# Performance work log

Measured on AMD Instinct MI355X. Metric: run time of the kernel, lower is better.

## Reference

```python
import jax, jax.numpy as jnp
import numpy as np

K = 4  # Chebyshev filter size (matches init_kwargs k)


def setup_inputs() -> dict:
    key = jax.random.key(0)
    ks = jax.random.split(key, 5)
    N, E, F_IN, F_OUT = 100000, 3200000, 128, 128
    signal = jax.random.normal(ks[0], (N, F_IN), dtype=jnp.float32)
    src = jax.random.randint(ks[1], (E,), 0, N, dtype=jnp.int32)
    dst = jax.random.randint(ks[2], (E,), 0, N, dtype=jnp.int32)
    W = jax.random.normal(ks[3], (F_OUT, F_IN * K), dtype=jnp.float32) * 0.02
    b = jax.random.normal(ks[4], (F_OUT,), dtype=jnp.float32) * 0.02
    lambda_max = jnp.ones((1,), dtype=jnp.float32) * 2.0
    return {"signal": signal, "src": src, "dst": dst, "W": W, "b": b,
            "lambda_max": lambda_max}


def reference(signal, src, dst, W, b, lambda_max):
    N = signal.shape[0]
    # in-degrees: number of edges landing on each node
    deg = jax.ops.segment_sum(jnp.ones_like(dst, dtype=signal.dtype), dst,
                              num_segments=N)
    d_sqrt = jnp.clip(deg, 1.0, None) ** -0.5  # [N]
    d_sqrt = d_sqrt[:, None]                   # [N, 1]

    def unn_laplacian(x):
        # D^{-1/2} A D^{-1/2} x via gather-scatter over edges
        msg = (x * d_sqrt)[src]                               # [E, F]
        agg = jax.ops.segment_sum(msg, dst, num_segments=N)   # [N, F]
        return agg * d_sqrt

    re_norm = 2.0 / lambda_max  # [1], broadcasts over [N, F]

    X0 = signal
    Xt = [X0]
    if K > 1:
        h = unn_laplacian(X0)
        X1 = -re_norm * h + X0 * (re_norm - 1.0)
        Xt.append(X1)
        for _ in range(2, K):
            h = unn_laplacian(X1)
            Xi = -2.0 * re_norm * h + X1 * 2.0 * (re_norm - 1.0) - X0
            Xt.append(Xi)
            X1, X0 = Xi, X1
    feats = jnp.concatenate(Xt, axis=-1)  # [N, K*F_in]
    return feats @ W.T + b
```

## Files before the change

### kernel.cpp

```cpp
#include <hip/hip_runtime.h>

#define FEAT 128
#define YS 8.0f
#define YIS 0.125f
#define BSHIFT 7
#define MAXB 1024
#define BIN_CH 8192
#define CAP 8192

typedef __attribute__((ext_vector_type(8))) short bf16x8;
typedef __attribute__((ext_vector_type(4))) float f32x4;

__device__ __forceinline__ float2 upk_bf2(unsigned int p) {
    union { unsigned int u; float f; } a, b;
    a.u = p << 16;
    b.u = p & 0xffff0000u;
    return make_float2(a.f, b.f);
}
__device__ __forceinline__ unsigned short f2bf(float f) {
    union { float f; unsigned int u; } v;
    v.f = f;
    unsigned int b = v.u + 0x7fffu + ((v.u >> 16) & 1u);
    return (unsigned short)(b >> 16);
}
__device__ __forceinline__ unsigned int pk_bf2(float x, float y) {
    return (unsigned int)f2bf(x) | ((unsigned int)f2bf(y) << 16);
}

__global__ __launch_bounds__(1024) void bin_kernel(const int* __restrict__ src,
                                                   const int* __restrict__ dst,
                                                   int* __restrict__ bcnt,
                                                   unsigned int* __restrict__ tmp,
                                                   int E, int NB) {
    __shared__ int cnt[MAXB];
    __shared__ int base[MAXB];
    int t = threadIdx.x;
    for (int i = t; i < NB; i += 1024) cnt[i] = 0;
    __syncthreads();
    int start = blockIdx.x * BIN_CH;
    int n = E - start;
    if (n > BIN_CH) n = BIN_CH;
    for (int k = t; k < n; k += 1024) atomicAdd(&cnt[dst[start + k] >> BSHIFT], 1);
    __syncthreads();
    for (int i = t; i < NB; i += 1024) {
        int c = cnt[i];
        base[i] = c ? atomicAdd(&bcnt[i], c) : 0;
        cnt[i] = 0;
    }
    __syncthreads();
    for (int k = t; k < n; k += 1024) {
        int s = src[start + k], d = dst[start + k];
        int b = d >> BSHIFT;
        int off = atomicAdd(&cnt[b], 1);
        tmp[(size_t)b * CAP + base[b] + off] =
            ((unsigned int)(d & 127) << 24) | (unsigned int)s;
    }
}

__global__ __launch_bounds__(256) void bucket_kernel(
    const unsigned int* __restrict__ tmp, const int* __restrict__ bcnt,
    float* __restrict__ dsq, int* __restrict__ rstart, int* __restrict__ rend,
    int* __restrict__ ssrc, int N) {
    __shared__ int ldeg[128];
    __shared__ int lofs[128];
    int b = blockIdx.x;
    int t = threadIdx.x;
    int cnt = bcnt[b];
    if (t < 128) ldeg[t] = 0;
    __syncthreads();
    const unsigned int* tp = tmp + (size_t)b * CAP;
    for (int e = t; e < cnt; e += 256) atomicAdd(&ldeg[tp[e] >> 24], 1);
    __syncthreads();
    int node = (b << BSHIFT) + t;
    int v = 0, pv = 0;
    if (t < 128 && node < N) {
        v = ldeg[t];
        pv = (v + 7) & ~7;
    }
    if (t < 128) lofs[t] = pv;
    __syncthreads();
    for (int off = 1; off < 128; off <<= 1) {
        int add = (t < 128 && t >= off) ? lofs[t - off] : 0;
        __syncthreads();
        if (t < 128) lofs[t] += add;
        __syncthreads();
    }
    int myStart = 0;
    if (t < 128) {
        myStart = lofs[t] - pv;
        if (node < N) {
            dsq[node] = rsqrtf((float)(v < 1 ? 1 : v));
            rstart[node] = b * CAP + myStart;
            rend[node] = b * CAP + lofs[t];
        }
        ldeg[t] = myStart;
    }
    __syncthreads();
    int* sp = ssrc + (size_t)b * CAP;
    for (int e = t; e < cnt; e += 256) {
        unsigned int p = tp[e];
        int dl = p >> 24;
        int pos = atomicAdd(&ldeg[dl], 1);
        sp[pos] = (int)(p & 0xFFFFFFu);
    }
    __syncthreads();
    if (t < 128 && node < N) {
        for (int p = myStart + v; p < myStart + pv; p++) sp[p] = N;
    }
}

__global__ void prep_kernel(const float* __restrict__ signal, const float* __restrict__ dsq,
                            unsigned int* __restrict__ X0b, unsigned short* __restrict__ y0,
                            unsigned short* __restrict__ y1, int total ) {
    int t = blockIdx.x * blockDim.x + threadIdx.x;
    if (t < 64) {
        y0[total + t] = 0;
        y1[total + t] = 0;
    }
    if (t >= total) return;
    int node = t >> 6;
    float2 v = ((const float2*)signal)[t];
    float ds = dsq[node];
    X0b[t] = pk_bf2(v.x, v.y);
    int p = __builtin_amdgcn_cvt_pk_fp8_f32(v.x * ds * YS, v.y * ds * YS, 0, false);
    y0[t] = (unsigned short)p;
}

__global__ void wconv_kernel(const float* __restrict__ W, unsigned int* __restrict__ Wb2,
                             int total ) {
    int u = blockIdx.x * blockDim.x + threadIdx.x;
    if (u >= total) return;
    int e2 = u & 3;
    int l15 = (u >> 2) & 15;
    int kg = (u >> 6) & 3;
    int kq = (u >> 8) & 3;
    int chunk = (u >> 10) & 3;
    int nt = (u >> 12) & 7;
    int col = nt * 16 + l15;
    int k = chunk * 128 + kq * 32 + kg * 8 + e2 * 2;
    float2 v = ((const float2*)W)[col * 256 + (k >> 1)];
    Wb2[u] = pk_bf2(v.x, v.y);
}

__global__ __launch_bounds__(256) void pull_combine_kernel(
    const unsigned short* __restrict__ y8, const int* __restrict__ rstart,
    const int* __restrict__ rend, const int* __restrict__ ssrc,
    const float* __restrict__ dsq, const unsigned int* __restrict__ xprev,
    const unsigned int* __restrict__ xpp, const float* __restrict__ lam,
    unsigned int* __restrict__ Xout, unsigned short* __restrict__ yout,
    int N, int mode) {
    int node = (blockIdx.x << 2) + (threadIdx.x >> 6);
    if (node >= N) return;
    int lane = threadIdx.x & 63;
    int i = __builtin_amdgcn_readfirstlane(rstart[node]);
    int end = __builtin_amdgcn_readfirstlane(rend[node]);
    float ax = 0.f, ay = 0.f;
    for (; i < end; i += 8) {
        int s[8];
#pragma unroll
        for (int j = 0; j < 8; j++) s[j] = __builtin_amdgcn_readfirstlane(ssrc[i + j]);
        unsigned int u[8];
#pragma unroll
        for (int j = 0; j < 8; j++) u[j] = y8[(size_t)s[j] * 64 + lane];
#pragma unroll
        for (int j = 0; j < 8; j++) {
            auto f = __builtin_amdgcn_cvt_pk_f32_fp8((int)u[j], false);
            ax += f[0];
            ay += f[1];
        }
    }
    float r = 2.0f / lam[0];
    float ds = dsq[node];
    size_t idx = (size_t)node * 64 + lane;
    float2 xp = upk_bf2(xprev[idx]);
    float rx, ry;
    if (mode == 1) {
        float alpha = -r * ds * YIS, beta = r - 1.0f;
        rx = alpha * ax + beta * xp.x;
        ry = alpha * ay + beta * xp.y;
    } else {
        float alpha = -2.0f * r * ds * YIS, beta = 2.0f * (r - 1.0f);
        float2 xq = upk_bf2(xpp[idx]);
        rx = alpha * ax + beta * xp.x - xq.x;
        ry = alpha * ay + beta * xp.y - xq.y;
    }
    Xout[idx] = pk_bf2(rx, ry);
    if (yout) {
        int p = __builtin_amdgcn_cvt_pk_fp8_f32(rx * ds * YS, ry * ds * YS, 0, false);
        yout[idx] = (unsigned short)p;
    }
}

__global__ __launch_bounds__(256, 4) void mfma_gemm_kernel(
    const unsigned short* __restrict__ X0, const unsigned short* __restrict__ X1,
    const unsigned short* __restrict__ X2, const unsigned short* __restrict__ X3,
    const unsigned short* __restrict__ Wb2, const float* __restrict__ bias,
    float* __restrict__ out, int M) {
    int tid = threadIdx.x;
    int lane = tid & 63;
    int w = tid >> 6;
    int m0 = blockIdx.x * 128 + w * 32;
    int l15 = lane & 15;
    int kg = lane >> 4;

    f32x4 acc[2][8];
#pragma unroll
    for (int rg = 0; rg < 2; rg++)
#pragma unroll
        for (int nt = 0; nt < 8; nt++) acc[rg][nt] = (f32x4)(0.f);

    const unsigned short* Xs[4] = {X0, X1, X2, X3};
    int arow[2];
#pragma unroll
    for (int rg = 0; rg < 2; rg++) {
        int r = m0 + rg * 16 + l15;
        arow[rg] = r < M ? r : M - 1;
    }
    const unsigned short* wlane = Wb2 + (kg * 16 + l15) * 8;

#pragma unroll
    for (int chunk = 0; chunk < 4; ++chunk) {
        const unsigned short* A = Xs[chunk];
#pragma unroll
        for (int kq = 0; kq < 4; kq++) {
            bf16x8 af[2];
#pragma unroll
            for (int rg = 0; rg < 2; rg++)
                af[rg] = *(const bf16x8*)(A + (size_t)arow[rg] * 128 + kq * 32 + kg * 8);
#pragma unroll
            for (int nt = 0; nt < 8; nt++) {
                bf16x8 bf = *(const bf16x8*)(wlane + nt * 8192 + chunk * 2048 + kq * 512);
#pragma unroll
                for (int rg = 0; rg < 2; rg++)
                    acc[rg][nt] = __builtin_amdgcn_mfma_f32_16x16x32_bf16(af[rg], bf,
                                                                          acc[rg][nt], 0, 0, 0);
            }
        }
    }
#pragma unroll
    for (int nt = 0; nt < 8; nt++) {
        int col = nt * 16 + l15;
        float bb = bias[col];
#pragma unroll
        for (int rg = 0; rg < 2; rg++) {
#pragma unroll
            for (int r = 0; r < 4; r++) {
                int row = m0 + rg * 16 + kg * 4 + r;
                if (row < M) out[(size_t)row * 128 + col] = acc[rg][nt][r] + bb;
            }
        }
    }
}

extern "C" void kernel_launch(void* const* d_in, const int* in_sizes, int n_in,
                              void* d_out, int out_size, void* d_ws, size_t ws_size,
                              hipStream_t stream) {
    const float* signal = (const float*)d_in[0];
    const int* src = (const int*)d_in[1];
    const int* dst = (const int*)d_in[2];
    const float* W = (const float*)d_in[3];
    const float* bias = (const float*)d_in[4];
    const float* lam = (const float*)d_in[5];
    int N = in_sizes[0] / FEAT;
    int E = in_sizes[1];
    float* out = (float*)d_out;
    int NB = (N + (1 << BSHIFT) - 1) >> BSHIFT;

    char* ws = (char*)d_ws;
    size_t off = 0;
    auto alloc = [&](size_t bytes) {
        char* p = ws + off;
        off += (bytes + 511) & ~(size_t)511;
        return p;
    };
    size_t nodeBf = (size_t)N * FEAT * 2;
    size_t nodeF8 = (size_t)(N + 1) * FEAT;
    size_t bucketBytes = (size_t)NB * CAP * 4;

    float* dsq = (float*)alloc((size_t)N * 4);
    int* bcnt = (int*)alloc((size_t)NB * 4);
    int* rstart = (int*)alloc((size_t)N * 4);
    int* rend = (int*)alloc((size_t)N * 4);
    int* ssrc = (int*)alloc(bucketBytes);
    unsigned int* tmp = (unsigned int*)alloc(bucketBytes);
    unsigned int* Wb = (unsigned int*)alloc((size_t)128 * 512 * 2);
    unsigned int* X0b = (unsigned int*)alloc(nodeBf);
    unsigned int* X1b = (unsigned int*)alloc(nodeBf);
    unsigned int* X2b = (unsigned int*)alloc(nodeBf);
    unsigned short* yA = (unsigned short*)alloc(nodeF8);
    unsigned short* yB = (unsigned short*)alloc(nodeF8);
    unsigned int* X3b = tmp;

    hipMemsetAsync(bcnt, 0, (size_t)NB * 4, stream);
    bin_kernel<<<(E + BIN_CH - 1) / BIN_CH, 1024, 0, stream>>>(src, dst, bcnt, tmp, E, NB);
    bucket_kernel<<<NB, 256, 0, stream>>>(tmp, bcnt, dsq, rstart, rend, ssrc, N);

    int tot64 = N * 64;
    prep_kernel<<<(tot64 + 255) / 256, 256, 0, stream>>>(signal, dsq, X0b, yA, yB, tot64);
    wconv_kernel<<<(32768 + 255) / 256, 256, 0, stream>>>(W, Wb, 32768);

    int pullBlocks = (N + 3) / 4;
    pull_combine_kernel<<<pullBlocks, 256, 0, stream>>>(yA, rstart, rend, ssrc, dsq,
                                                        X0b, X0b, lam, X1b, yB, N, 1);
    pull_combine_kernel<<<pullBlocks, 256, 0, stream>>>(yB, rstart, rend, ssrc, dsq,
                                                        X1b, X0b, lam, X2b, yA, N, 2);
    pull_combine_kernel<<<pullBlocks, 256, 0, stream>>>(yA, rstart, rend, ssrc, dsq,
                                                        X2b, X1b, lam, X3b, nullptr, N, 2);

    mfma_gemm_kernel<<<(N + 127) / 128, 256, 0, stream>>>(
        (const unsigned short*)X0b, (const unsigned short*)X1b,
        (const unsigned short*)X2b, (const unsigned short*)X3b,
        (const unsigned short*)Wb, bias, out, N);
}
```

Measured before the change: 360.7 us.

## Widen dst buckets to 256 nodes and unroll pull gather by 16

Buckets now hold 256 destination nodes with a larger per-bucket capacity, and each node's edge list is padded to a multiple of 16 instead of 8. The pull kernel reads source indices as int4 vector loads and issues 16 independent fp8 row gathers per iteration, aiming for more memory-level parallelism and fewer loop iterations. The cost is more padding edges (extra dummy gathers of the zero row), higher register use, and fewer, larger binning buckets. CAP of 16384 per 256-node bucket sits close to the expected edge count per bucket, so there is less headroom against overflow.

Measured after the change: 344.3 us, median of 2. 4.5% less time.

```diff
diff --git a/kernel.cpp b/kernel.cpp
--- a/kernel.cpp
+++ b/kernel.cpp
@@ -3,10 +3,10 @@
 #define FEAT 128
 #define YS 8.0f
 #define YIS 0.125f
-#define BSHIFT 7
-#define MAXB 1024
+#define BSHIFT 8
+#define NBMAX 512
 #define BIN_CH 8192
-#define CAP 8192
+#define CAP 16384
 
 typedef __attribute__((ext_vector_type(8))) short bf16x8;
 typedef __attribute__((ext_vector_type(4))) float f32x4;
@@ -32,8 +32,8 @@
                                                    int* __restrict__ bcnt,
                                                    unsigned int* __restrict__ tmp,
                                                    int E, int NB) {
-    __shared__ int cnt[MAXB];
-    __shared__ int base[MAXB];
+    __shared__ int cnt[NBMAX];
+    __shared__ int base[NBMAX];
     int t = threadIdx.x;
     for (int i = t; i < NB; i += 1024) cnt[i] = 0;
     __syncthreads();
@@ -53,7 +53,7 @@
         int b = d >> BSHIFT;
         int off = atomicAdd(&cnt[b], 1);
         tmp[(size_t)b * CAP + base[b] + off] =
-            ((unsigned int)(d & 127) << 24) | (unsigned int)s;
+            ((unsigned int)(d & 255) << 24) | (unsigned int)s;
     }
 }
 
@@ -61,40 +61,37 @@
     const unsigned int* __restrict__ tmp, const int* __restrict__ bcnt,
     float* __restrict__ dsq, int* __restrict__ rstart, int* __restrict__ rend,
     int* __restrict__ ssrc, int N) {
-    __shared__ int ldeg[128];
-    __shared__ int lofs[128];
+    __shared__ int ldeg[256];
+    __shared__ int lofs[256];
     int b = blockIdx.x;
     int t = threadIdx.x;
     int cnt = bcnt[b];
-    if (t < 128) ldeg[t] = 0;
+    ldeg[t] = 0;
     __syncthreads();
     const unsigned int* tp = tmp + (size_t)b * CAP;
     for (int e = t; e < cnt; e += 256) atomicAdd(&ldeg[tp[e] >> 24], 1);
     __syncthreads();
     int node = (b << BSHIFT) + t;
     int v = 0, pv = 0;
-    if (t < 128 && node < N) {
+    if (node < N) {
         v = ldeg[t];
-        pv = (v + 7) & ~7;
-    }
-    if (t < 128) lofs[t] = pv;
-    __syncthreads();
-    for (int off = 1; off < 128; off <<= 1) {
-        int add = (t < 128 && t >= off) ? lofs[t - off] : 0;
+        pv = (v + 15) & ~15;
+    }
+    lofs[t] = pv;
+    __syncthreads();
+    for (int off = 1; off < 256; off <<= 1) {
+        int add = (t >= off) ? lofs[t - off] : 0;
         __syncthreads();
-        if (t < 128) lofs[t] += add;
+        lofs[t] += add;
         __syncthreads();
     }
-    int myStart = 0;
-    if (t < 128) {
-        myStart = lofs[t] - pv;
-        if (node < N) {
-            dsq[node] = rsqrtf((float)(v < 1 ? 1 : v));
-            rstart[node] = b * CAP + myStart;
-            rend[node] = b * CAP + lofs[t];
-        }
-        ldeg[t] = myStart;
-    }
+    int myStart = lofs[t] - pv;
+    if (node < N) {
+        dsq[node] = rsqrtf((float)(v < 1 ? 1 : v));
+        rstart[node] = b * CAP + myStart;
+        rend[node] = b * CAP + lofs[t];
+    }
+    ldeg[t] = myStart;
     __syncthreads();
     int* sp = ssrc + (size_t)b * CAP;
     for (int e = t; e < cnt; e += 256) {
@@ -104,7 +101,7 @@
         sp[pos] = (int)(p & 0xFFFFFFu);
     }
     __syncthreads();
-    if (t < 128 && node < N) {
+    if (node < N) {
         for (int p = myStart + v; p < myStart + pv; p++) sp[p] = N;
     }
 }
@@ -155,15 +152,33 @@
     int i = __builtin_amdgcn_readfirstlane(rstart[node]);
     int end = __builtin_amdgcn_readfirstlane(rend[node]);
     float ax = 0.f, ay = 0.f;
-    for (; i < end; i += 8) {
-        int s[8];
-#pragma unroll
-        for (int j = 0; j < 8; j++) s[j] = __builtin_amdgcn_readfirstlane(ssrc[i + j]);
-        unsigned int u[8];
-#pragma unroll
-        for (int j = 0; j < 8; j++) u[j] = y8[(size_t)s[j] * 64 + lane];
-#pragma unroll
-        for (int j = 0; j < 8; j++) {
+    for (; i < end; i += 16) {
+        int4 sa = *(const int4*)(ssrc + i);
+        int4 sb = *(const int4*)(ssrc + i + 4);
+        int4 sc = *(const int4*)(ssrc + i + 8);
+        int4 sd = *(const int4*)(ssrc + i + 12);
+        int s[16];
+        s[0] = __builtin_amdgcn_readfirstlane(sa.x);
+        s[1] = __builtin_amdgcn_readfirstlane(sa.y);
+        s[2] = __builtin_amdgcn_readfirstlane(sa.z);
+        s[3] = __builtin_amdgcn_readfirstlane(sa.w);
+        s[4] = __builtin_amdgcn_readfirstlane(sb.x);
+        s[5] = __builtin_amdgcn_readfirstlane(sb.y);
+        s[6] = __builtin_amdgcn_readfirstlane(sb.z);
+        s[7] = __builtin_amdgcn_readfirstlane(sb.w);
+        s[8] = __builtin_amdgcn_readfirstlane(sc.x);
+        s[9] = __builtin_amdgcn_readfirstlane(sc.y);
+        s[10] = __builtin_amdgcn_readfirstlane(sc.z);
+        s[11] = __builtin_amdgcn_readfirstlane(sc.w);
+        s[12] = __builtin_amdgcn_readfirstlane(sd.x);
+        s[13] = __builtin_amdgcn_readfirstlane(sd.y);
+        s[14] = __builtin_amdgcn_readfirstlane(sd.z);
+        s[15] = __builtin_amdgcn_readfirstlane(sd.w);
+        unsigned int u[16];
+#pragma unroll
+        for (int j = 0; j < 16; j++) u[j] = y8[(size_t)s[j] * 64 + lane];
+#pragma unroll
+        for (int j = 0; j < 16; j++) {
             auto f = __builtin_amdgcn_cvt_pk_f32_fp8((int)u[j], false);
             ax += f[0];
             ay += f[1];
```
